# Kernel tuning notes

Hardware: AMD Instinct MI355X
Metric: run time of the kernel (lower is better)

## Reference

```python
import jax, jax.numpy as jnp
import numpy as np

B, NQ, NKV = 4, 1024, 2048
DQ, DC, DI, H = 1024, 1024, 1024, 16
DH = DI // H
EPS = 1e-5


def layer_norm(x, gamma, beta):
    mu = jnp.mean(x, axis=-1, keepdims=True)
    var = jnp.var(x, axis=-1, keepdims=True)
    return (x - mu) * jax.lax.rsqrt(var + EPS) * gamma + beta


def setup_inputs() -> dict:
    key = jax.random.key(0)
    ks = jax.random.split(key, 6)
    s = 0.02
    return {
        "q": jax.random.normal(ks[0], (B, NQ, DQ), jnp.float32),
        "context": jax.random.normal(ks[1], (B, NKV, DC), jnp.float32),
        "Wq": jax.random.normal(ks[2], (DI, DQ), jnp.float32) * s,
        "Wkv": jax.random.normal(ks[3], (2 * DI, DC), jnp.float32) * s,
        "Wproj": jax.random.normal(ks[4], (DQ, DI), jnp.float32) * s,
        "bproj": jnp.zeros((DQ,), jnp.float32),
        "q_gamma": jnp.ones((DQ,), jnp.float32),
        "q_beta": jnp.zeros((DQ,), jnp.float32),
        "c_gamma": jnp.ones((DC,), jnp.float32),
        "c_beta": jnp.zeros((DC,), jnp.float32),
    }


def reference(q, context, Wq, Wkv, Wproj, bproj, q_gamma, q_beta, c_gamma, c_beta):
    scale = DH ** -0.5
    qn = layer_norm(q, q_gamma, q_beta)            # [b, nq, dq]
    cn = layer_norm(context, c_gamma, c_beta)      # [b, nkv, dc]
    qp = qn @ Wq.T                                  # [b, nq, di]
    kv = cn @ Wkv.T                                 # [b, nkv, 2*di]
    k, v = kv[..., :DI], kv[..., DI:]
    qh = qp.reshape(B, NQ, H, DH)
    kh = k.reshape(B, NKV, H, DH)
    vh = v.reshape(B, NKV, H, DH)
    attn = jnp.einsum('bnhd,bmhd->bhnm', qh, kh) * scale   # [b,h,nq,nkv]
    attn = jax.nn.softmax(attn, axis=-1)
    out = jnp.einsum('bhnm,bmhd->bnhd', attn, vh).reshape(B, NQ, DI)
    return out @ Wproj.T + bproj
```

## Files before the change

kernel.cpp:

```cpp
#include <hip/hip_runtime.h>
#include <hip/hip_bf16.h>
#include <stdint.h>

#define B_N 4
#define NQ 1024
#define NKV 2048
#define DI 1024
#define H 16
#define DH 64

using bf16 = __bf16;
typedef bf16 bf16x8 __attribute__((ext_vector_type(8)));
typedef bf16 bf16x4 __attribute__((ext_vector_type(4)));
typedef float f32x4 __attribute__((ext_vector_type(4)));

typedef const __attribute__((address_space(1))) void* gptr_t;
typedef __attribute__((address_space(3))) void* sptr_t;

__global__ __launch_bounds__(256) void cvt_kernel(const float* __restrict__ in,
                                                  bf16* __restrict__ out, int n4) {
  int i = blockIdx.x * blockDim.x + threadIdx.x;
  if (i < n4) {
    float4 v = reinterpret_cast<const float4*>(in)[i];
    bf16x4 o;
    o[0] = (bf16)v.x; o[1] = (bf16)v.y; o[2] = (bf16)v.z; o[3] = (bf16)v.w;
    reinterpret_cast<bf16x4*>(out)[i] = o;
  }
}

__global__ __launch_bounds__(256) void ln_kernel(const float* __restrict__ x,
    const float* __restrict__ gamma, const float* __restrict__ beta,
    bf16* __restrict__ out) {
  int row = blockIdx.x;
  int t = threadIdx.x;
  const float4 v = reinterpret_cast<const float4*>(x + (size_t)row * 1024)[t];
  float s = v.x + v.y + v.z + v.w;
  float s2 = v.x*v.x + v.y*v.y + v.z*v.z + v.w*v.w;
#pragma unroll
  for (int m = 1; m < 64; m <<= 1) { s += __shfl_xor(s, m); s2 += __shfl_xor(s2, m); }
  __shared__ float red[8];
  int wid = t >> 6;
  if ((t & 63) == 0) { red[wid] = s; red[wid + 4] = s2; }
  __syncthreads();
  float ts  = red[0] + red[1] + red[2] + red[3];
  float ts2 = red[4] + red[5] + red[6] + red[7];
  float mean = ts * (1.0f / 1024.0f);
  float var  = ts2 * (1.0f / 1024.0f) - mean * mean;
  float rstd = rsqrtf(var + 1e-5f);
  float4 g  = reinterpret_cast<const float4*>(gamma)[t];
  float4 bb = reinterpret_cast<const float4*>(beta)[t];
  bf16x4 o;
  o[0] = (bf16)((v.x - mean) * rstd * g.x + bb.x);
  o[1] = (bf16)((v.y - mean) * rstd * g.y + bb.y);
  o[2] = (bf16)((v.z - mean) * rstd * g.z + bb.z);
  o[3] = (bf16)((v.w - mean) * rstd * g.w + bb.w);
  reinterpret_cast<bf16x4*>(out + (size_t)row * 1024)[t] = o;
}

template<int MODE, int BN>
__global__ __launch_bounds__(256) void gemm_bt(const bf16* __restrict__ A,
    const bf16* __restrict__ Bm, void* __restrict__ out0, void* __restrict__ out1,
    const float* __restrict__ bias, int M, int N) {
  constexpr int K = 1024;
  constexpr int MI = (BN == 128) ? 4 : 2;
  __shared__ bf16 lA[128 * 32];
  __shared__ bf16 lB[BN * 32];
  const int nbn = N / BN;
  const int bm = blockIdx.x / nbn, bn = blockIdx.x - bm * nbn;
  const int m0 = bm << 7, n0 = bn * BN;
  const int tid = threadIdx.x;
  const int lane = tid & 63, wid = tid >> 6;
  const int rowb = (BN == 128) ? ((wid >> 1) * 64) : (wid * 32);
  const int colb = (BN == 128) ? ((wid & 1) * 64) : 0;
  const int l15 = lane & 15, lg = lane >> 4;

  f32x4 acc[MI][4] = {};

  const int c0 = tid, c1 = tid + 256;
  const bf16* gA0 = A  + (size_t)(m0 + (c0 >> 2)) * K + ((c0 & 3) << 3);
  const bf16* gA1 = A  + (size_t)(m0 + (c1 >> 2)) * K + ((c1 & 3) << 3);
  const bf16* gB0 = Bm + (size_t)(n0 + (c0 >> 2)) * K + ((c0 & 3) << 3);
  const bf16* gB1 = Bm + (size_t)(n0 + (c1 >> 2)) * K + ((c1 & 3) << 3);

  for (int k0 = 0; k0 < K; k0 += 32) {
    __builtin_amdgcn_global_load_lds((gptr_t)(gA0 + k0), (sptr_t)(lA + c0 * 8), 16, 0, 0);
    __builtin_amdgcn_global_load_lds((gptr_t)(gA1 + k0), (sptr_t)(lA + c1 * 8), 16, 0, 0);
    __builtin_amdgcn_global_load_lds((gptr_t)(gB0 + k0), (sptr_t)(lB + c0 * 8), 16, 0, 0);
    if constexpr (BN == 128)
      __builtin_amdgcn_global_load_lds((gptr_t)(gB1 + k0), (sptr_t)(lB + c1 * 8), 16, 0, 0);
    __syncthreads();
    bf16x8 af[MI], bfr[4];
#pragma unroll
    for (int i = 0; i < MI; ++i)
      af[i]  = *reinterpret_cast<const bf16x8*>(lA + (rowb + i * 16 + l15) * 32 + lg * 8);
#pragma unroll
    for (int j = 0; j < 4; ++j)
      bfr[j] = *reinterpret_cast<const bf16x8*>(lB + (colb + j * 16 + l15) * 32 + lg * 8);
#pragma unroll
    for (int i = 0; i < MI; ++i)
#pragma unroll
      for (int j = 0; j < 4; ++j)
        acc[i][j] = __builtin_amdgcn_mfma_f32_16x16x32_bf16(af[i], bfr[j], acc[i][j], 0, 0, 0);
    __syncthreads();
  }

  const int mB = m0 + rowb + lg * 4;
  const int nB = n0 + colb + l15;
  if constexpr (MODE == 0) {
    bf16* o = reinterpret_cast<bf16*>(out0);
    constexpr float SC = 0.125f * 1.44269504089f;
#pragma unroll
    for (int i = 0; i < MI; ++i)
#pragma unroll
      for (int j = 0; j < 4; ++j)
#pragma unroll
        for (int r = 0; r < 4; ++r)
          o[(size_t)(mB + i * 16 + r) * N + nB + j * 16] = (bf16)(acc[i][j][r] * SC);
  } else if constexpr (MODE == 2) {
    float* o = reinterpret_cast<float*>(out0);
#pragma unroll
    for (int j = 0; j < 4; ++j) {
      float bj = bias[nB + j * 16];
#pragma unroll
      for (int i = 0; i < MI; ++i)
#pragma unroll
        for (int r = 0; r < 4; ++r)
          o[(size_t)(mB + i * 16 + r) * N + nB + j * 16] = acc[i][j][r] + bj;
    }
  } else {
    if (n0 < 1024) {
      bf16* o = reinterpret_cast<bf16*>(out0);
#pragma unroll
      for (int i = 0; i < MI; ++i)
#pragma unroll
        for (int j = 0; j < 4; ++j)
#pragma unroll
          for (int r = 0; r < 4; ++r)
            o[(size_t)(mB + i * 16 + r) * 1024 + nB + j * 16] = (bf16)acc[i][j][r];
    } else {
      bf16* o = reinterpret_cast<bf16*>(out1);
#pragma unroll
      for (int i = 0; i < MI; ++i) {
        int m = mB + i * 16;
        int bb_ = m >> 11, kv = m & 2047;
        int u = kv & 63;
        int c = (u & 32) | ((u & 12) << 1) | ((u & 16) >> 2) | (u & 3);
        int col = (kv & ~63) | c;
#pragma unroll
        for (int j = 0; j < 4; ++j) {
          int nv = nB + j * 16 - 1024;
          bf16x4 pk;
          pk[0] = (bf16)acc[i][j][0]; pk[1] = (bf16)acc[i][j][1];
          pk[2] = (bf16)acc[i][j][2]; pk[3] = (bf16)acc[i][j][3];
          *reinterpret_cast<bf16x4*>(o + ((size_t)(bb_ << 10) + nv) * 2048 + col) = pk;
        }
      }
    }
  }
}

__global__ __launch_bounds__(512) void attn_kernel(const bf16* __restrict__ qp,
    const bf16* __restrict__ kk, const bf16* __restrict__ vTp, bf16* __restrict__ out) {
  __shared__ bf16 smem[16384];
  const int pos = blockIdx.x;
  const int idx = pos >> 3;
  const int bh = ((idx >> 3) << 3) | (pos & 7);
  const int qt = idx & 7;
  const int b = bh >> 4, h = bh & 15;
  const int tid = threadIdx.x;
  const int lane = tid & 63, w = tid >> 6;
  const int l15 = lane & 15, lg = lane >> 4;

  const bf16* Qb = qp + (size_t)(b * NQ + qt * 128 + w * 16) * DI + h * DH;
  const bf16* Kb = kk + (size_t)b * NKV * DI + h * DH;
  const bf16* Vb = vTp + (size_t)(b * DI + h * DH) * NKV;

  const int r0 = ((tid >> 7) << 4) | (tid & 15);
  const int c0_ = (tid >> 4) & 7;
  const bf16* pK0 = Kb + (size_t)r0 * DI + c0_ * 8;
  const bf16* pV0 = Vb + (size_t)r0 * NKV + c0_ * 8;

#define STAGE_KV(bufsel, kv)                                                                       \
  do {                                                                                             \
    __builtin_amdgcn_global_load_lds((gptr_t)(pK0 + (size_t)(kv) * DI),                            \
                                     (sptr_t)(smem + (bufsel) * 4096 + tid * 8), 16, 0, 0);        \
    __builtin_amdgcn_global_load_lds((gptr_t)(pV0 + (kv)),                                         \
                                     (sptr_t)(smem + 8192 + (bufsel) * 4096 + tid * 8), 16, 0, 0); \
  } while (0)

  bf16x8 qf[2];
#pragma unroll
  for (int ks = 0; ks < 2; ++ks)
    qf[ks] = *reinterpret_cast<const bf16x8*>(Qb + (size_t)l15 * DI + ks * 32 + lg * 8);

  f32x4 o[4] = {};
  float mrun = -1e30f;
  float lpart = 0.0f;

  STAGE_KV(0, 0);
  __syncthreads();
  int cur = 0;

  for (int kv0 = 0; kv0 < NKV; kv0 += 64) {
    const bool notlast = (kv0 + 64 < NKV);
    if (notlast) STAGE_KV(cur ^ 1, kv0 + 64);

    const bf16* Kl = smem + cur * 4096;
    const bf16* Vl = smem + 8192 + cur * 4096;
    bf16x8 kf[4][2], vf[4][2];
#pragma unroll
    for (int ni = 0; ni < 4; ++ni)
#pragma unroll
      for (int ks = 0; ks < 2; ++ks)
        kf[ni][ks] = *reinterpret_cast<const bf16x8*>(Kl + ((ni * 2 + ks) * 64 + lane) * 8);
#pragma unroll
    for (int dt = 0; dt < 4; ++dt)
#pragma unroll
      for (int k2 = 0; k2 < 2; ++k2)
        vf[dt][k2] = *reinterpret_cast<const bf16x8*>(Vl + ((dt * 2 + k2) * 64 + lane) * 8);

    f32x4 s[4] = {};
    __builtin_amdgcn_s_setprio(1);
#pragma unroll
    for (int ni = 0; ni < 4; ++ni)
#pragma unroll
      for (int ks = 0; ks < 2; ++ks)
        s[ni] = __builtin_amdgcn_mfma_f32_16x16x32_bf16(kf[ni][ks], qf[ks], s[ni], 0, 0, 0);
    __builtin_amdgcn_s_setprio(0);

    float pm;
    {
      float m0_ = fmaxf(fmaxf(s[0][0], s[0][1]), fmaxf(s[0][2], s[0][3]));
      float m1_ = fmaxf(fmaxf(s[1][0], s[1][1]), fmaxf(s[1][2], s[1][3]));
      float m2_ = fmaxf(fmaxf(s[2][0], s[2][1]), fmaxf(s[2][2], s[2][3]));
      float m3_ = fmaxf(fmaxf(s[3][0], s[3][1]), fmaxf(s[3][2], s[3][3]));
      pm = fmaxf(fmaxf(m0_, m1_), fmaxf(m2_, m3_));
    }
    pm = fmaxf(pm, __shfl_xor(pm, 16));
    pm = fmaxf(pm, __shfl_xor(pm, 32));

    const bool noresc = __all(pm <= mrun);
    const float mnew = noresc ? mrun : fmaxf(mrun, pm);

    float rsn[4];
#pragma unroll
    for (int ni = 0; ni < 4; ++ni) {
#pragma unroll
      for (int r = 0; r < 4; ++r)
        s[ni][r] = __builtin_amdgcn_exp2f(s[ni][r] - mnew);
      rsn[ni] = (s[ni][0] + s[ni][1]) + (s[ni][2] + s[ni][3]);
    }
    const float rs_local = (rsn[0] + rsn[1]) + (rsn[2] + rsn[3]);

    if (noresc) {
      lpart += rs_local;
    } else {
      float corr = __builtin_amdgcn_exp2f(mrun - mnew);
      lpart = lpart * corr + rs_local;
      mrun = mnew;
      float c0 = __shfl(corr, lg * 4 + 0);
      float c1 = __shfl(corr, lg * 4 + 1);
      float c2 = __shfl(corr, lg * 4 + 2);
      float c3 = __shfl(corr, lg * 4 + 3);
#pragma unroll
      for (int dt = 0; dt < 4; ++dt) {
        o[dt][0] *= c0; o[dt][1] *= c1; o[dt][2] *= c2; o[dt][3] *= c3;
      }
    }

    bf16x8 pa0, pa1;
#pragma unroll
    for (int jj = 0; jj < 4; ++jj) {
      pa0[jj]     = (bf16)s[0][jj];
      pa0[4 + jj] = (bf16)s[1][jj];
      pa1[jj]     = (bf16)s[2][jj];
      pa1[4 + jj] = (bf16)s[3][jj];
    }
    __builtin_amdgcn_s_setprio(1);
#pragma unroll
    for (int dt = 0; dt < 4; ++dt)
      o[dt] = __builtin_amdgcn_mfma_f32_16x16x32_bf16(pa0, vf[dt][0], o[dt], 0, 0, 0);
#pragma unroll
    for (int dt = 0; dt < 4; ++dt)
      o[dt] = __builtin_amdgcn_mfma_f32_16x16x32_bf16(pa1, vf[dt][1], o[dt], 0, 0, 0);
    __builtin_amdgcn_s_setprio(0);

    if (notlast) __syncthreads();
    cur ^= 1;
  }
#undef STAGE_KV

  float lsum = lpart;
  lsum += __shfl_xor(lsum, 16);
  lsum += __shfl_xor(lsum, 32);
  const float inv = 1.0f / lsum;
  const float iv0 = __shfl(inv, lg * 4 + 0);
  const float iv1 = __shfl(inv, lg * 4 + 1);
  const float iv2 = __shfl(inv, lg * 4 + 2);
  const float iv3 = __shfl(inv, lg * 4 + 3);

  bf16* Ob = out + (size_t)(b * NQ + qt * 128 + w * 16) * DI + h * DH;
#pragma unroll
  for (int dt = 0; dt < 4; ++dt) {
    Ob[(size_t)(lg * 4 + 0) * DI + dt * 16 + l15] = (bf16)(o[dt][0] * iv0);
    Ob[(size_t)(lg * 4 + 1) * DI + dt * 16 + l15] = (bf16)(o[dt][1] * iv1);
    Ob[(size_t)(lg * 4 + 2) * DI + dt * 16 + l15] = (bf16)(o[dt][2] * iv2);
    Ob[(size_t)(lg * 4 + 3) * DI + dt * 16 + l15] = (bf16)(o[dt][3] * iv3);
  }
}

extern "C" void kernel_launch(void* const* d_in, const int* in_sizes, int n_in,
                              void* d_out, int out_size, void* d_ws, size_t ws_size,
                              hipStream_t stream) {
  const float* q     = (const float*)d_in[0];
  const float* ctx   = (const float*)d_in[1];
  const float* Wq    = (const float*)d_in[2];
  const float* Wkv   = (const float*)d_in[3];
  const float* Wproj = (const float*)d_in[4];
  const float* bproj = (const float*)d_in[5];
  const float* qg    = (const float*)d_in[6];
  const float* qb    = (const float*)d_in[7];
  const float* cg    = (const float*)d_in[8];
  const float* cb    = (const float*)d_in[9];

  char* ws = (char*)d_ws;
  bf16* qn    = (bf16*)(ws);
  bf16* cn    = (bf16*)(ws + ( 8ull << 20));
  bf16* Wq_b  = (bf16*)(ws + (24ull << 20));
  bf16* Wkv_b = (bf16*)(ws + (26ull << 20));
  bf16* Wp_b  = (bf16*)(ws + (30ull << 20));
  bf16* qpb   = (bf16*)(ws + (32ull << 20));
  bf16* kbuf  = (bf16*)(ws + (40ull << 20));
  bf16* vT    = (bf16*)(ws + (56ull << 20));
  bf16* aout  = (bf16*)(ws + (72ull << 20));

  cvt_kernel<<<1024, 256, 0, stream>>>(Wq,    Wq_b,  (1024 * 1024) / 4);
  cvt_kernel<<<2048, 256, 0, stream>>>(Wkv,   Wkv_b, (2048 * 1024) / 4);
  cvt_kernel<<<1024, 256, 0, stream>>>(Wproj, Wp_b,  (1024 * 1024) / 4);
  ln_kernel<<<4096, 256, 0, stream>>>(q,   qg, qb, qn);
  ln_kernel<<<8192, 256, 0, stream>>>(ctx, cg, cb, cn);

  gemm_bt<0, 64><<<512,  256, 0, stream>>>(qn,   Wq_b,  qpb,  nullptr, nullptr, 4096, 1024);
  gemm_bt<1,128><<<1024, 256, 0, stream>>>(cn,   Wkv_b, kbuf, vT,      nullptr, 8192, 2048);

  attn_kernel<<<512, 512, 0, stream>>>(qpb, kbuf, vT, aout);

  gemm_bt<2, 64><<<512,  256, 0, stream>>>(aout, Wp_b,  d_out, nullptr, bproj, 4096, 1024);
}
```

Before: 173.0 us.

## Merge prep launches, deepen GEMM K-tile to 64, double attention KV tile to 128

The three weight-conversion launches become one kernel, and the two layernorm launches become one, which cuts launch overhead. The GEMM K step grows from 32 to 64, halving the number of barriers and loop iterations per output tile at the cost of twice the LDS. The attention kernel stages 128 KV rows per iteration instead of 64, with 64KB of LDS and a launch bound of 4 blocks. This halves the sync and online-softmax bookkeeping per key, but LDS use and register pressure go up, which may limit occupancy.

```diff
diff --git a/kernel.cpp b/kernel.cpp
--- a/kernel.cpp
+++ b/kernel.cpp
@@ -17,23 +17,31 @@
 typedef const __attribute__((address_space(1))) void* gptr_t;
 typedef __attribute__((address_space(3))) void* sptr_t;
 
-__global__ __launch_bounds__(256) void cvt_kernel(const float* __restrict__ in,
-                                                  bf16* __restrict__ out, int n4) {
-  int i = blockIdx.x * blockDim.x + threadIdx.x;
-  if (i < n4) {
-    float4 v = reinterpret_cast<const float4*>(in)[i];
-    bf16x4 o;
-    o[0] = (bf16)v.x; o[1] = (bf16)v.y; o[2] = (bf16)v.z; o[3] = (bf16)v.w;
-    reinterpret_cast<bf16x4*>(out)[i] = o;
-  }
-}
-
-__global__ __launch_bounds__(256) void ln_kernel(const float* __restrict__ x,
-    const float* __restrict__ gamma, const float* __restrict__ beta,
-    bf16* __restrict__ out) {
+__global__ __launch_bounds__(256) void cvt_all(const float* __restrict__ Wq,
+    const float* __restrict__ Wkv, const float* __restrict__ Wproj,
+    bf16* __restrict__ oq, bf16* __restrict__ okv, bf16* __restrict__ op) {
+  int i = blockIdx.x * 256 + threadIdx.x;
+  const float* src; bf16* dst; int j;
+  if (i < 262144)      { src = Wq;    dst = oq;  j = i; }
+  else if (i < 786432) { src = Wkv;   dst = okv; j = i - 262144; }
+  else                 { src = Wproj; dst = op;  j = i - 786432; }
+  float4 v = reinterpret_cast<const float4*>(src)[j];
+  bf16x4 o;
+  o[0] = (bf16)v.x; o[1] = (bf16)v.y; o[2] = (bf16)v.z; o[3] = (bf16)v.w;
+  reinterpret_cast<bf16x4*>(dst)[j] = o;
+}
+
+__global__ __launch_bounds__(256) void ln_kernel(const float* __restrict__ q,
+    const float* __restrict__ ctx,
+    const float* __restrict__ qg, const float* __restrict__ qb,
+    const float* __restrict__ cg, const float* __restrict__ cb,
+    bf16* __restrict__ qn, bf16* __restrict__ cn) {
   int row = blockIdx.x;
+  const float* x; const float* gamma; const float* beta; bf16* out; int r;
+  if (row < 4096) { x = q;   gamma = qg; beta = qb; out = qn; r = row; }
+  else            { x = ctx; gamma = cg; beta = cb; out = cn; r = row - 4096; }
   int t = threadIdx.x;
-  const float4 v = reinterpret_cast<const float4*>(x + (size_t)row * 1024)[t];
+  const float4 v = reinterpret_cast<const float4*>(x + (size_t)r * 1024)[t];
   float s = v.x + v.y + v.z + v.w;
   float s2 = v.x*v.x + v.y*v.y + v.z*v.z + v.w*v.w;
 #pragma unroll
@@ -54,7 +62,7 @@
   o[1] = (bf16)((v.y - mean) * rstd * g.y + bb.y);
   o[2] = (bf16)((v.z - mean) * rstd * g.z + bb.z);
   o[3] = (bf16)((v.w - mean) * rstd * g.w + bb.w);
-  reinterpret_cast<bf16x4*>(out + (size_t)row * 1024)[t] = o;
+  reinterpret_cast<bf16x4*>(out + (size_t)r * 1024)[t] = o;
 }
 
 template<int MODE, int BN>
@@ -63,8 +71,9 @@
     const float* __restrict__ bias, int M, int N) {
   constexpr int K = 1024;
   constexpr int MI = (BN == 128) ? 4 : 2;
-  __shared__ bf16 lA[128 * 32];
-  __shared__ bf16 lB[BN * 32];
+  constexpr int NBL = (BN == 128) ? 4 : 2;
+  __shared__ bf16 lA[128 * 64];
+  __shared__ bf16 lB[BN * 64];
   const int nbn = N / BN;
   const int bm = blockIdx.x / nbn, bn = blockIdx.x - bm * nbn;
   const int m0 = bm << 7, n0 = bn * BN;
@@ -76,31 +85,41 @@
 
   f32x4 acc[MI][4] = {};
 
-  const int c0 = tid, c1 = tid + 256;
-  const bf16* gA0 = A  + (size_t)(m0 + (c0 >> 2)) * K + ((c0 & 3) << 3);
-  const bf16* gA1 = A  + (size_t)(m0 + (c1 >> 2)) * K + ((c1 & 3) << 3);
-  const bf16* gB0 = Bm + (size_t)(n0 + (c0 >> 2)) * K + ((c0 & 3) << 3);
-  const bf16* gB1 = Bm + (size_t)(n0 + (c1 >> 2)) * K + ((c1 & 3) << 3);
-
-  for (int k0 = 0; k0 < K; k0 += 32) {
-    __builtin_amdgcn_global_load_lds((gptr_t)(gA0 + k0), (sptr_t)(lA + c0 * 8), 16, 0, 0);
-    __builtin_amdgcn_global_load_lds((gptr_t)(gA1 + k0), (sptr_t)(lA + c1 * 8), 16, 0, 0);
-    __builtin_amdgcn_global_load_lds((gptr_t)(gB0 + k0), (sptr_t)(lB + c0 * 8), 16, 0, 0);
-    if constexpr (BN == 128)
-      __builtin_amdgcn_global_load_lds((gptr_t)(gB1 + k0), (sptr_t)(lB + c1 * 8), 16, 0, 0);
+  const bf16* gA[4]; const bf16* gB[NBL];
+#pragma unroll
+  for (int u = 0; u < 4; ++u) {
+    int s = tid + u * 256;
+    gA[u] = A + (size_t)(m0 + (s >> 3)) * K + ((s & 7) << 3);
+  }
+#pragma unroll
+  for (int u = 0; u < NBL; ++u) {
+    int s = tid + u * 256;
+    gB[u] = Bm + (size_t)(n0 + (s >> 3)) * K + ((s & 7) << 3);
+  }
+
+  for (int k0 = 0; k0 < K; k0 += 64) {
+#pragma unroll
+    for (int u = 0; u < 4; ++u)
+      __builtin_amdgcn_global_load_lds((gptr_t)(gA[u] + k0), (sptr_t)(lA + (tid + u * 256) * 8), 16, 0, 0);
+#pragma unroll
+    for (int u = 0; u < NBL; ++u)
+      __builtin_amdgcn_global_load_lds((gptr_t)(gB[u] + k0), (sptr_t)(lB + (tid + u * 256) * 8), 16, 0, 0);
     __syncthreads();
-    bf16x8 af[MI], bfr[4];
-#pragma unroll
-    for (int i = 0; i < MI; ++i)
-      af[i]  = *reinterpret_cast<const bf16x8*>(lA + (rowb + i * 16 + l15) * 32 + lg * 8);
-#pragma unroll
-    for (int j = 0; j < 4; ++j)
-      bfr[j] = *reinterpret_cast<const bf16x8*>(lB + (colb + j * 16 + l15) * 32 + lg * 8);
-#pragma unroll
-    for (int i = 0; i < MI; ++i)
+#pragma unroll
+    for (int ks2 = 0; ks2 < 2; ++ks2) {
+      bf16x8 af[MI], bfr[4];
+#pragma unroll
+      for (int i = 0; i < MI; ++i)
+        af[i]  = *reinterpret_cast<const bf16x8*>(lA + (rowb + i * 16 + l15) * 64 + ks2 * 32 + lg * 8);
 #pragma unroll
       for (int j = 0; j < 4; ++j)
-        acc[i][j] = __builtin_amdgcn_mfma_f32_16x16x32_bf16(af[i], bfr[j], acc[i][j], 0, 0, 0);
+        bfr[j] = *reinterpret_cast<const bf16x8*>(lB + (colb + j * 16 + l15) * 64 + ks2 * 32 + lg * 8);
+#pragma unroll
+      for (int i = 0; i < MI; ++i)
+#pragma unroll
+        for (int j = 0; j < 4; ++j)
+          acc[i][j] = __builtin_amdgcn_mfma_f32_16x16x32_bf16(af[i], bfr[j], acc[i][j], 0, 0, 0);
+    }
     __syncthreads();
   }
 
@@ -159,9 +178,9 @@
   }
 }
 
-__global__ __launch_bounds__(512) void attn_kernel(const bf16* __restrict__ qp,
+__global__ __launch_bounds__(512, 4) void attn_kernel(const bf16* __restrict__ qp,
     const bf16* __restrict__ kk, const bf16* __restrict__ vTp, bf16* __restrict__ out) {
-  __shared__ bf16 smem[16384];
+  __shared__ bf16 smem[32768];
   const int pos = blockIdx.x;
   const int idx = pos >> 3;
   const int bh = ((idx >> 3) << 3) | (pos & 7);
@@ -175,17 +194,26 @@
   const bf16* Kb = kk + (size_t)b * NKV * DI + h * DH;
   const bf16* Vb = vTp + (size_t)(b * DI + h * DH) * NKV;
 
-  const int r0 = ((tid >> 7) << 4) | (tid & 15);
-  const int c0_ = (tid >> 4) & 7;
-  const bf16* pK0 = Kb + (size_t)r0 * DI + c0_ * 8;
-  const bf16* pV0 = Vb + (size_t)r0 * NKV + c0_ * 8;
-
-#define STAGE_KV(bufsel, kv)                                                                       \
-  do {                                                                                             \
-    __builtin_amdgcn_global_load_lds((gptr_t)(pK0 + (size_t)(kv) * DI),                            \
-                                     (sptr_t)(smem + (bufsel) * 4096 + tid * 8), 16, 0, 0);        \
-    __builtin_amdgcn_global_load_lds((gptr_t)(pV0 + (kv)),                                         \
-                                     (sptr_t)(smem + 8192 + (bufsel) * 4096 + tid * 8), 16, 0, 0); \
+  const int sA = tid, sB = tid + 512;
+  const int rKA = ((sA >> 7) << 4) | (sA & 15), cKA = ((sA >> 4) & 7) * 8;
+  const int rKB = ((sB >> 7) << 4) | (sB & 15), cKB = ((sB >> 4) & 7) * 8;
+  const int rVA = ((sA >> 8) << 4) | (sA & 15), cVA = ((sA >> 6) & 3) * 32 + ((sA >> 4) & 3) * 8;
+  const int rVB = ((sB >> 8) << 4) | (sB & 15), cVB = ((sB >> 6) & 3) * 32 + ((sB >> 4) & 3) * 8;
+  const bf16* pKA = Kb + (size_t)rKA * DI + cKA;
+  const bf16* pKB = Kb + (size_t)rKB * DI + cKB;
+  const bf16* pVA = Vb + (size_t)rVA * NKV + cVA;
+  const bf16* pVB = Vb + (size_t)rVB * NKV + cVB;
+
+#define STAGE_KV(bufsel, kv)                                                                        \
+  do {                                                                                              \
+    __builtin_amdgcn_global_load_lds((gptr_t)(pKA + (size_t)(kv) * DI),                             \
+                                     (sptr_t)(smem + (bufsel) * 8192 + sA * 8), 16, 0, 0);          \
+    __builtin_amdgcn_global_load_lds((gptr_t)(pKB + (size_t)(kv) * DI),                             \
+                                     (sptr_t)(smem + (bufsel) * 8192 + sB * 8), 16, 0, 0);          \
+    __builtin_amdgcn_global_load_lds((gptr_t)(pVA + (kv)),                                          \
+                                     (sptr_t)(smem + 16384 + (bufsel) * 8192 + sA * 8), 16, 0, 0);  \
+    __builtin_amdgcn_global_load_lds((gptr_t)(pVB + (kv)),                                          \
+                                     (sptr_t)(smem + 16384 + (bufsel) * 8192 + sB * 8), 16, 0, 0);  \
   } while (0)
 
   bf16x8 qf[2];
@@ -201,56 +229,54 @@
   __syncthreads();
   int cur = 0;
 
-  for (int kv0 = 0; kv0 < NKV; kv0 += 64) {
-    const bool notlast = (kv0 + 64 < NKV);
-    if (notlast) STAGE_KV(cur ^ 1, kv0 + 64);
-
-    const bf16* Kl = smem + cur * 4096;
-    const bf16* Vl = smem + 8192 + cur * 4096;
-    bf16x8 kf[4][2], vf[4][2];
-#pragma unroll
-    for (int ni = 0; ni < 4; ++ni)
-#pragma unroll
-      for (int ks = 0; ks < 2; ++ks)
-        kf[ni][ks] = *reinterpret_cast<const bf16x8*>(Kl + ((ni * 2 + ks) * 64 + lane) * 8);
-#pragma unroll
-    for (int dt = 0; dt < 4; ++dt)
-#pragma unroll
-      for (int k2 = 0; k2 < 2; ++k2)
-        vf[dt][k2] = *reinterpret_cast<const bf16x8*>(Vl + ((dt * 2 + k2) * 64 + lane) * 8);
-
-    f32x4 s[4] = {};
-    __builtin_amdgcn_s_setprio(1);
-#pragma unroll
-    for (int ni = 0; ni < 4; ++ni)
-#pragma unroll
-      for (int ks = 0; ks < 2; ++ks)
-        s[ni] = __builtin_amdgcn_mfma_f32_16x16x32_bf16(kf[ni][ks], qf[ks], s[ni], 0, 0, 0);
-    __builtin_amdgcn_s_setprio(0);
-
-    float pm;
-    {
-      float m0_ = fmaxf(fmaxf(s[0][0], s[0][1]), fmaxf(s[0][2], s[0][3]));
-      float m1_ = fmaxf(fmaxf(s[1][0], s[1][1]), fmaxf(s[1][2], s[1][3]));
-      float m2_ = fmaxf(fmaxf(s[2][0], s[2][1]), fmaxf(s[2][2], s[2][3]));
-      float m3_ = fmaxf(fmaxf(s[3][0], s[3][1]), fmaxf(s[3][2], s[3][3]));
-      pm = fmaxf(fmaxf(m0_, m1_), fmaxf(m2_, m3_));
-    }
+  for (int kv0 = 0; kv0 < NKV; kv0 += 128) {
+    const bool notlast = (kv0 + 128 < NKV);
+    if (notlast) STAGE_KV(cur ^ 1, kv0 + 128);
+
+    const bf16* Kl = smem + cur * 8192;
+    const bf16* Vl = smem + 16384 + cur * 8192;
+
+    f32x4 s[8] = {};
+#pragma unroll
+    for (int h2 = 0; h2 < 2; ++h2) {
+      bf16x8 kf[4][2];
+#pragma unroll
+      for (int ni = 0; ni < 4; ++ni)
+#pragma unroll
+        for (int ks = 0; ks < 2; ++ks)
+          kf[ni][ks] = *reinterpret_cast<const bf16x8*>(Kl + (((h2 * 4 + ni) * 2 + ks) * 64 + lane) * 8);
+      __builtin_amdgcn_s_setprio(1);
+#pragma unroll
+      for (int ni = 0; ni < 4; ++ni)
+#pragma unroll
+        for (int ks = 0; ks < 2; ++ks)
+          s[h2 * 4 + ni] = __builtin_amdgcn_mfma_f32_16x16x32_bf16(kf[ni][ks], qf[ks], s[h2 * 4 + ni], 0, 0, 0);
+      __builtin_amdgcn_s_setprio(0);
+    }
+
+    f32x4 mv = s[0];
+#pragma unroll
+    for (int i = 1; i < 8; ++i) {
+      mv[0] = fmaxf(mv[0], s[i][0]); mv[1] = fmaxf(mv[1], s[i][1]);
+      mv[2] = fmaxf(mv[2], s[i][2]); mv[3] = fmaxf(mv[3], s[i][3]);
+    }
+    float pm = fmaxf(fmaxf(mv[0], mv[1]), fmaxf(mv[2], mv[3]));
     pm = fmaxf(pm, __shfl_xor(pm, 16));
     pm = fmaxf(pm, __shfl_xor(pm, 32));
 
     const bool noresc = __all(pm <= mrun);
     const float mnew = noresc ? mrun : fmaxf(mrun, pm);
 
-    float rsn[4];
-#pragma unroll
-    for (int ni = 0; ni < 4; ++ni) {
-#pragma unroll
-      for (int r = 0; r < 4; ++r)
-        s[ni][r] = __builtin_amdgcn_exp2f(s[ni][r] - mnew);
-      rsn[ni] = (s[ni][0] + s[ni][1]) + (s[ni][2] + s[ni][3]);
-    }
-    const float rs_local = (rsn[0] + rsn[1]) + (rsn[2] + rsn[3]);
+    f32x4 sv = {};
+#pragma unroll
+    for (int i = 0; i < 8; ++i) {
+#pragma unroll
+      for (int r = 0; r < 4; ++r) {
+        s[i][r] = __builtin_amdgcn_exp2f(s[i][r] - mnew);
+        sv[r] += s[i][r];
+      }
+    }
+    const float rs_local = (sv[0] + sv[1]) + (sv[2] + sv[3]);
 
     if (noresc) {
       lpart += rs_local;
@@ -268,21 +294,28 @@
       }
     }
 
-    bf16x8 pa0, pa1;
-#pragma unroll
-    for (int jj = 0; jj < 4; ++jj) {
-      pa0[jj]     = (bf16)s[0][jj];
-      pa0[4 + jj] = (bf16)s[1][jj];
-      pa1[jj]     = (bf16)s[2][jj];
-      pa1[4 + jj] = (bf16)s[3][jj];
-    }
+    bf16x8 pa[4];
+#pragma unroll
+    for (int h2 = 0; h2 < 2; ++h2)
+#pragma unroll
+      for (int k2p = 0; k2p < 2; ++k2p)
+#pragma unroll
+        for (int jj = 0; jj < 4; ++jj) {
+          pa[h2 * 2 + k2p][jj]     = (bf16)s[h2 * 4 + k2p * 2 + 0][jj];
+          pa[h2 * 2 + k2p][4 + jj] = (bf16)s[h2 * 4 + k2p * 2 + 1][jj];
+        }
+
     __builtin_amdgcn_s_setprio(1);
 #pragma unroll
-    for (int dt = 0; dt < 4; ++dt)
-      o[dt] = __builtin_amdgcn_mfma_f32_16x16x32_bf16(pa0, vf[dt][0], o[dt], 0, 0, 0);
-#pragma unroll
-    for (int dt = 0; dt < 4; ++dt)
-      o[dt] = __builtin_amdgcn_mfma_f32_16x16x32_bf16(pa1, vf[dt][1], o[dt], 0, 0, 0);
+    for (int k2 = 0; k2 < 4; ++k2) {
+      bf16x8 vf[4];
+#pragma unroll
+      for (int dt = 0; dt < 4; ++dt)
+        vf[dt] = *reinterpret_cast<const bf16x8*>(Vl + ((dt * 4 + k2) * 64 + lane) * 8);
+#pragma unroll
+      for (int dt = 0; dt < 4; ++dt)
+        o[dt] = __builtin_amdgcn_mfma_f32_16x16x32_bf16(pa[k2], vf[dt], o[dt], 0, 0, 0);
+    }
     __builtin_amdgcn_s_setprio(0);
 
     if (notlast) __syncthreads();
@@ -334,11 +367,8 @@
   bf16* vT    = (bf16*)(ws + (56ull << 20));
   bf16* aout  = (bf16*)(ws + (72ull << 20));
 
-  cvt_kernel<<<1024, 256, 0, stream>>>(Wq,    Wq_b,  (1024 * 1024) / 4);
-  cvt_kernel<<<2048, 256, 0, stream>>>(Wkv,   Wkv_b, (2048 * 1024) / 4);
-  cvt_kernel<<<1024, 256, 0, stream>>>(Wproj, Wp_b,  (1024 * 1024) / 4);
-  ln_kernel<<<4096, 256, 0, stream>>>(q,   qg, qb, qn);
-  ln_kernel<<<8192, 256, 0, stream>>>(ctx, cg, cb, cn);
+  cvt_all<<<4096, 256, 0, stream>>>(Wq, Wkv, Wproj, Wq_b, Wkv_b, Wp_b);
+  ln_kernel<<<12288, 256, 0, stream>>>(q, ctx, qg, qb, cg, cb, qn, cn);
 
   gemm_bt<0, 64><<<512,  256, 0, stream>>>(qn,   Wq_b,  qpb,  nullptr, nullptr, 4096, 1024);
   gemm_bt<1,128><<<1024, 256, 0, stream>>>(cn,   Wkv_b, kbuf, vT,      nullptr, 8192, 2048);
```

Result: faster. 163.8 us (-5.3%).
